# Performance work log

Measured on AMD Instinct MI355X. Metric: run time of the kernel, lower is better.

The kernel has to match this reference:

```python
import jax, jax.numpy as jnp
import numpy as np

N_NODES = 100000
N_EDGES = 640000
D = 128
EPS = 1e-5

def _full_layer_norm(x):
    # torch layer_norm with normalized_shape == x.shape: stats over ALL elements
    mu = jnp.mean(x)
    var = jnp.mean(jnp.square(x - mu))  # biased variance
    return (x - mu) * jax.lax.rsqrt(var + EPS)

def setup_inputs() -> dict:
    key = jax.random.key(0)
    k1, k2, k3, k4, k5 = jax.random.split(key, 5)
    scale1 = 1.0 / np.sqrt(D)
    scale2 = 1.0 / np.sqrt(2 * D)
    return {
        "edge_features": jax.random.normal(k1, (N_EDGES, D), dtype=jnp.float32),
        "node_features": jax.random.normal(k2, (N_NODES, D), dtype=jnp.float32),
        "edge_indices": jax.random.randint(k3, (N_EDGES, 2), 0, N_NODES, dtype=jnp.int32),
        "W1": jax.random.normal(k4, (D, D), dtype=jnp.float32) * scale1,
        "b1": jnp.zeros((D,), dtype=jnp.float32),
        "W2": jax.random.normal(k5, (2 * D, D), dtype=jnp.float32) * scale2,
        "b2": jnp.zeros((D,), dtype=jnp.float32),
    }

def reference(edge_features, node_features, edge_indices, W1, b1, W2, b2):
    # node MLP: linear -> whole-tensor layernorm -> gelu
    h = node_features @ W1 + b1                       # [N, D]
    h = jax.nn.gelu(_full_layer_norm(h), approximate=False)
    # gather source-node features onto edges
    src = edge_indices[:, 0]
    dst = edge_indices[:, 1]
    gathered = h[src]                                 # [E, D]
    e = jnp.concatenate([edge_features, gathered], axis=1)  # [E, 2D]
    e = e @ W2 + b2                                   # [E, D]
    e = jax.nn.gelu(_full_layer_norm(e), approximate=False)
    # scatter-mean (include_self=False): nodes with no in-edges stay 0
    seg_sum = jax.ops.segment_sum(e, dst, num_segments=N_NODES)       # [N, D]
    counts = jax.ops.segment_sum(jnp.ones((e.shape[0],), e.dtype), dst,
                                 num_segments=N_NODES)                 # [N]
    counts = counts[:, None]
    return jnp.where(counts > 0, seg_sum / jnp.maximum(counts, 1.0), 0.0)
```

## Files before the change

### kernel.cpp

```cpp
#include <hip/hip_runtime.h>
#include <hip/hip_bf16.h>
#include <math.h>

typedef __bf16 bf16;
typedef bf16 bf16x8 __attribute__((ext_vector_type(8)));
typedef float f32x4 __attribute__((ext_vector_type(4)));
typedef unsigned short ushort_t;
typedef unsigned long long u64;

#define N_NODES 100000
#define N_EDGES 640000
#define DD 128
#define MAXDEG 64
#define STAT_SCALE 1048576.0

__device__ __forceinline__ float gelu_fast(float x) {
    float z2 = x * (1.595769122f + 0.071354816f * x * x);
    return x * __builtin_amdgcn_rcpf(1.0f + __expf(-z2));
}

__device__ __forceinline__ ushort_t bf16_bits(float x) {
    bf16 h = (bf16)x;
    return __builtin_bit_cast(ushort_t, h);
}

__device__ __forceinline__ float bits_to_f(ushort_t u) {
    return __uint_as_float(((unsigned)u) << 16);
}

__device__ __forceinline__ long long to_fixed(double x) {
    return (long long)(x * STAT_SCALE + (x >= 0.0 ? 0.5 : -0.5));
}

__device__ __forceinline__ void stats_atomic(float lsum, float lsq, float* red,
                                             u64* dsum, u64* dsq) {
    int tid = threadIdx.x;
    red[tid] = lsum; __syncthreads();
    for (int s = 128; s > 0; s >>= 1) { if (tid < s) red[tid] += red[tid + s]; __syncthreads(); }
    float bs = red[0]; __syncthreads();
    red[tid] = lsq; __syncthreads();
    for (int s = 128; s > 0; s >>= 1) { if (tid < s) red[tid] += red[tid + s]; __syncthreads(); }
    if (tid == 0) {
        atomicAdd(dsum, (u64)to_fixed((double)bs));
        atomicAdd(dsq,  (u64)to_fixed((double)red[0]));
    }
}

__device__ __forceinline__ void stats_decode(const u64* stats, double cnt,
                                             float* mu, float* rs) {
    long long ss = (long long)stats[0], sq = (long long)stats[1];
    double mu_d = ((double)ss / STAT_SCALE) / cnt;
    double var  = ((double)sq / STAT_SCALE) / cnt - mu_d * mu_d;
    *mu = (float)mu_d;
    *rs = (float)(1.0 / sqrt(var + 1e-5));
}

#define K1_TILES 1563
__global__ __launch_bounds__(256) void k1_gemm1(
    const float* __restrict__ nf, const float* __restrict__ W1,
    const float* __restrict__ b1, ushort_t* __restrict__ hpre,
    u64* __restrict__ stats, int nblocks)
{
    __shared__ bf16 Ash[64 * 136];
    __shared__ float red[256];
    const int tid = threadIdx.x;
    const int lane = tid & 63;
    const int w = tid >> 6;
    const int l15 = lane & 15, l4 = lane >> 4;

    bf16x8 bfrag[4][2];
    #pragma unroll
    for (int s = 0; s < 4; ++s)
        #pragma unroll
        for (int t = 0; t < 2; ++t) {
            int n = w * 32 + t * 16 + l15;
            #pragma unroll
            for (int j = 0; j < 8; ++j)
                bfrag[s][t][j] = (bf16)W1[(s * 32 + l4 * 8 + j) * DD + n];
        }
    float4 bias4[2];
    bias4[0] = *(const float4*)&b1[w * 32 + l4 * 4];
    bias4[1] = *(const float4*)&b1[w * 32 + 16 + l4 * 4];

    float lsum = 0.f, lsq = 0.f;
    const int srow = tid >> 2;
    const int q = tid & 3;

    for (int tile = blockIdx.x; tile < K1_TILES; tile += nblocks) {
        const int rbase = tile * 64;
        {
            int grow = min(rbase + srow, N_NODES - 1);
            const float4* p = (const float4*)&nf[(size_t)grow * DD + q * 32];
            #pragma unroll
            for (int u = 0; u < 4; ++u) {
                float4 a = p[2 * u], b = p[2 * u + 1];
                ushort_t o[8] = {bf16_bits(a.x), bf16_bits(a.y), bf16_bits(a.z), bf16_bits(a.w),
                                 bf16_bits(b.x), bf16_bits(b.y), bf16_bits(b.z), bf16_bits(b.w)};
                *(uint4*)&Ash[srow * 136 + q * 32 + u * 8] = *(const uint4*)o;
            }
        }
        __syncthreads();
        f32x4 acc[4][2];
        #pragma unroll
        for (int r = 0; r < 4; ++r)
            #pragma unroll
            for (int t = 0; t < 2; ++t)
                acc[r][t] = (f32x4){0.f, 0.f, 0.f, 0.f};
        #pragma unroll
        for (int s = 0; s < 4; ++s)
            #pragma unroll
            for (int r = 0; r < 4; ++r) {
                bf16x8 a = *(const bf16x8*)&Ash[(r * 16 + l15) * 136 + s * 32 + l4 * 8];
                acc[r][0] = __builtin_amdgcn_mfma_f32_16x16x32_bf16(bfrag[s][0], a, acc[r][0], 0, 0, 0);
                acc[r][1] = __builtin_amdgcn_mfma_f32_16x16x32_bf16(bfrag[s][1], a, acc[r][1], 0, 0, 0);
            }
        __syncthreads();
        #pragma unroll
        for (int r = 0; r < 4; ++r) {
            int row = rbase + r * 16 + l15;
            if (row < N_NODES) {
                #pragma unroll
                for (int t = 0; t < 2; ++t) {
                    int col = w * 32 + t * 16 + l4 * 4;
                    ushort_t o[4];
                    #pragma unroll
                    for (int j = 0; j < 4; ++j) {
                        float v = acc[r][t][j] + bias4[t][j];
                        lsum += v; lsq += v * v;
                        o[j] = bf16_bits(v);
                    }
                    *(uint2*)&hpre[(size_t)row * DD + col] = *(const uint2*)o;
                }
            }
        }
    }
    stats_atomic(lsum, lsq, red, &stats[0], &stats[1]);
}

__global__ __launch_bounds__(256) void k2b_gemmh(
    const ushort_t* __restrict__ hpre, const float* __restrict__ W2,
    const u64* __restrict__ stats, ushort_t* __restrict__ hh, int nblocks)
{
    __shared__ bf16 Ash[64 * 136];
    float mu, rs;
    stats_decode(stats, (double)N_NODES * DD, &mu, &rs);

    const int tid = threadIdx.x;
    const int lane = tid & 63;
    const int w = tid >> 6;
    const int l15 = lane & 15, l4 = lane >> 4;

    bf16x8 bfrag[4][2];
    #pragma unroll
    for (int s = 0; s < 4; ++s)
        #pragma unroll
        for (int t = 0; t < 2; ++t) {
            int n = w * 32 + t * 16 + l15;
            #pragma unroll
            for (int j = 0; j < 8; ++j)
                bfrag[s][t][j] = (bf16)W2[(DD + s * 32 + l4 * 8 + j) * DD + n];
        }

    const int srow = tid >> 2;
    const int q = tid & 3;

    for (int tile = blockIdx.x; tile < K1_TILES; tile += nblocks) {
        const int rbase = tile * 64;
        {
            int grow = min(rbase + srow, N_NODES - 1);
            const uint4* p = (const uint4*)&hpre[(size_t)grow * DD + q * 32];
            #pragma unroll
            for (int u = 0; u < 4; ++u) {
                uint4 v = p[u];
                const ushort_t* in = (const ushort_t*)&v;
                ushort_t o[8];
                #pragma unroll
                for (int j = 0; j < 8; ++j)
                    o[j] = bf16_bits(gelu_fast((bits_to_f(in[j]) - mu) * rs));
                *(uint4*)&Ash[srow * 136 + q * 32 + u * 8] = *(const uint4*)o;
            }
        }
        __syncthreads();
        f32x4 acc[4][2];
        #pragma unroll
        for (int r = 0; r < 4; ++r)
            #pragma unroll
            for (int t = 0; t < 2; ++t)
                acc[r][t] = (f32x4){0.f, 0.f, 0.f, 0.f};
        #pragma unroll
        for (int s = 0; s < 4; ++s)
            #pragma unroll
            for (int r = 0; r < 4; ++r) {
                bf16x8 a = *(const bf16x8*)&Ash[(r * 16 + l15) * 136 + s * 32 + l4 * 8];
                acc[r][0] = __builtin_amdgcn_mfma_f32_16x16x32_bf16(bfrag[s][0], a, acc[r][0], 0, 0, 0);
                acc[r][1] = __builtin_amdgcn_mfma_f32_16x16x32_bf16(bfrag[s][1], a, acc[r][1], 0, 0, 0);
            }
        __syncthreads();
        #pragma unroll
        for (int r = 0; r < 4; ++r) {
            int row = rbase + r * 16 + l15;
            if (row < N_NODES) {
                #pragma unroll
                for (int t = 0; t < 2; ++t) {
                    int col = w * 32 + t * 16 + l4 * 4;
                    ushort_t o[4];
                    #pragma unroll
                    for (int j = 0; j < 4; ++j)
                        o[j] = bf16_bits(acc[r][t][j]);
                    *(uint2*)&hh[(size_t)row * DD + col] = *(const uint2*)o;
                }
            }
        }
    }
}

__global__ __launch_bounds__(256) void k4_gemm2(
    const float* __restrict__ ef, const ushort_t* __restrict__ hh,
    const int* __restrict__ eidx, const float* __restrict__ W2,
    const float* __restrict__ b2, ushort_t* __restrict__ e0,
    u64* __restrict__ stats, int nblocks)
{
    __shared__ bf16 Ash[64 * 136];
    __shared__ int Ssrc[64];
    __shared__ float red[256];
    const int tid = threadIdx.x;
    const int lane = tid & 63;
    const int w = tid >> 6;
    const int l15 = lane & 15, l4 = lane >> 4;

    bf16x8 bfrag[4][2];
    #pragma unroll
    for (int s = 0; s < 4; ++s)
        #pragma unroll
        for (int t = 0; t < 2; ++t) {
            int n = w * 32 + t * 16 + l15;
            #pragma unroll
            for (int j = 0; j < 8; ++j)
                bfrag[s][t][j] = (bf16)W2[(s * 32 + l4 * 8 + j) * DD + n];
        }
    float4 bias4[2];
    bias4[0] = *(const float4*)&b2[w * 32 + l4 * 4];
    bias4[1] = *(const float4*)&b2[w * 32 + 16 + l4 * 4];

    float lsum = 0.f, lsq = 0.f;
    const int srow = tid >> 2;
    const int q = tid & 3;

    for (int tile = blockIdx.x; tile < N_EDGES / 64; tile += nblocks) {
        const int ebase = tile * 64;
        {
            const float4* p = (const float4*)&ef[(size_t)(ebase + srow) * DD + q * 32];
            #pragma unroll
            for (int u = 0; u < 4; ++u) {
                float4 a = p[2 * u], b = p[2 * u + 1];
                ushort_t o[8] = {bf16_bits(a.x), bf16_bits(a.y), bf16_bits(a.z), bf16_bits(a.w),
                                 bf16_bits(b.x), bf16_bits(b.y), bf16_bits(b.z), bf16_bits(b.w)};
                *(uint4*)&Ash[srow * 136 + q * 32 + u * 8] = *(const uint4*)o;
            }
            if (tid < 64) Ssrc[tid] = eidx[(size_t)(ebase + tid) * 2];
        }
        __syncthreads();
        f32x4 acc[4][2];
        #pragma unroll
        for (int r = 0; r < 4; ++r)
            #pragma unroll
            for (int t = 0; t < 2; ++t)
                acc[r][t] = (f32x4){0.f, 0.f, 0.f, 0.f};
        #pragma unroll
        for (int s = 0; s < 4; ++s)
            #pragma unroll
            for (int r = 0; r < 4; ++r) {
                bf16x8 a = *(const bf16x8*)&Ash[(r * 16 + l15) * 136 + s * 32 + l4 * 8];
                acc[r][0] = __builtin_amdgcn_mfma_f32_16x16x32_bf16(bfrag[s][0], a, acc[r][0], 0, 0, 0);
                acc[r][1] = __builtin_amdgcn_mfma_f32_16x16x32_bf16(bfrag[s][1], a, acc[r][1], 0, 0, 0);
            }
        int srows[4];
        #pragma unroll
        for (int r = 0; r < 4; ++r) srows[r] = Ssrc[r * 16 + l15];
        __syncthreads();
        #pragma unroll
        for (int r = 0; r < 4; ++r) {
            int row = ebase + r * 16 + l15;
            #pragma unroll
            for (int t = 0; t < 2; ++t) {
                int col = w * 32 + t * 16 + l4 * 4;
                uint2 hv = *(const uint2*)&hh[(size_t)srows[r] * DD + col];
                float h0 = bits_to_f((ushort_t)(hv.x & 0xffff));
                float h1 = bits_to_f((ushort_t)(hv.x >> 16));
                float h2 = bits_to_f((ushort_t)(hv.y & 0xffff));
                float h3 = bits_to_f((ushort_t)(hv.y >> 16));
                float hadd[4] = {h0, h1, h2, h3};
                ushort_t o[4];
                #pragma unroll
                for (int j = 0; j < 4; ++j) {
                    float v = acc[r][t][j] + bias4[t][j] + hadd[j];
                    lsum += v; lsq += v * v;
                    o[j] = bf16_bits(v);
                }
                *(uint2*)&e0[(size_t)row * DD + col] = *(const uint2*)o;
            }
        }
    }
    stats_atomic(lsum, lsq, red, &stats[2], &stats[3]);
}

__global__ __launch_bounds__(256) void k7_fill(
    const int* __restrict__ eidx, int* __restrict__ cnt, int* __restrict__ slot)
{
    int e = blockIdx.x * 256 + threadIdx.x;
    if (e >= N_EDGES) return;
    int dst = eidx[(size_t)e * 2 + 1];
    int pos = atomicAdd(&cnt[dst], 1);
    if (pos < MAXDEG) slot[dst * MAXDEG + pos] = e;
}

__global__ __launch_bounds__(256) void k8_gather(
    const ushort_t* __restrict__ e0v, const int* __restrict__ slot,
    const int* __restrict__ cnt, const u64* __restrict__ stats,
    float* __restrict__ out)
{
    float mu, rs;
    stats_decode(stats + 2, (double)N_EDGES * DD, &mu, &rs);
    int node = (int)((blockIdx.x * 256 + threadIdx.x) >> 6);
    int lane = threadIdx.x & 63;
    if (node >= N_NODES) return;
    int c = cnt[node];
    int m = min(c, MAXDEG);
    int myslot = (lane < m) ? slot[node * MAXDEG + lane] : 0;
    float a0 = 0.f, a1 = 0.f;
    const size_t off = (size_t)(lane * 2);
    int j = 0;
    for (; j + 4 <= m; j += 4) {
        int ea = __shfl(myslot, j);
        int eb = __shfl(myslot, j + 1);
        int ec = __shfl(myslot, j + 2);
        int ed = __shfl(myslot, j + 3);
        unsigned ua = *(const unsigned*)&e0v[(size_t)ea * DD + off];
        unsigned ub = *(const unsigned*)&e0v[(size_t)eb * DD + off];
        unsigned uc = *(const unsigned*)&e0v[(size_t)ec * DD + off];
        unsigned ud = *(const unsigned*)&e0v[(size_t)ed * DD + off];
        a0 += gelu_fast((__uint_as_float(ua << 16) - mu) * rs);
        a1 += gelu_fast((__uint_as_float(ua & 0xffff0000u) - mu) * rs);
        a0 += gelu_fast((__uint_as_float(ub << 16) - mu) * rs);
        a1 += gelu_fast((__uint_as_float(ub & 0xffff0000u) - mu) * rs);
        a0 += gelu_fast((__uint_as_float(uc << 16) - mu) * rs);
        a1 += gelu_fast((__uint_as_float(uc & 0xffff0000u) - mu) * rs);
        a0 += gelu_fast((__uint_as_float(ud << 16) - mu) * rs);
        a1 += gelu_fast((__uint_as_float(ud & 0xffff0000u) - mu) * rs);
    }
    for (; j < m; ++j) {
        int ea = __shfl(myslot, j);
        unsigned ua = *(const unsigned*)&e0v[(size_t)ea * DD + off];
        a0 += gelu_fast((__uint_as_float(ua << 16) - mu) * rs);
        a1 += gelu_fast((__uint_as_float(ua & 0xffff0000u) - mu) * rs);
    }
    float inv = c > 0 ? 1.0f / (float)c : 0.f;
    float2 res = {a0 * inv, a1 * inv};
    *(float2*)&out[(size_t)node * DD + lane * 2] = res;
}

extern "C" void kernel_launch(void* const* d_in, const int* in_sizes, int n_in,
                              void* d_out, int out_size, void* d_ws, size_t ws_size,
                              hipStream_t stream) {
    const float* ef  = (const float*)d_in[0];
    const float* nf  = (const float*)d_in[1];
    const int*   eix = (const int*)d_in[2];
    const float* W1  = (const float*)d_in[3];
    const float* b1  = (const float*)d_in[4];
    const float* W2  = (const float*)d_in[5];
    const float* b2  = (const float*)d_in[6];
    float* out = (float*)d_out;
    char* ws = (char*)d_ws;

    ushort_t* hpre  = (ushort_t*)(ws + 0);
    ushort_t* hh    = (ushort_t*)(ws + 25600000);
    ushort_t* e0    = (ushort_t*)(ws + 51200000);
    int*      cnt   = (int*)(ws + 215040000);
    u64*      stats = (u64*)(ws + 215440000);
    int*      slot  = (int*)(ws + 215440064);

    hipMemsetAsync(cnt, 0, 400064, stream);
    k1_gemm1<<<782, 256, 0, stream>>>(nf, W1, b1, hpre, stats, 782);
    k2b_gemmh<<<782, 256, 0, stream>>>(hpre, W2, stats, hh, 782);
    k7_fill<<<2500, 256, 0, stream>>>(eix, cnt, slot);
    k4_gemm2<<<2500, 256, 0, stream>>>(ef, hh, eix, W2, b2, e0, stats, 2500);
    k8_gather<<<25000, 256, 0, stream>>>(e0, slot, cnt, stats, out);
}
```

Measured before the change: 311.3 us.

## Register-prefetch next tile in GEMM kernels and hoist gather loads

The three GEMM kernels now software-pipeline their input tiles: the next tile's rows are loaded into registers while the current tile runs through MFMA, then packed into shared memory at the top of the next iteration. In k4, the source-index and hh-gather loads are issued at the start of each tile instead of after the MFMA loop, so their latency can overlap with compute. Grid sizes are reduced so each block processes several tiles and the prefetch has work to overlap with. The cost is extra register pressure from the prefetch buffers and fewer resident blocks.

New measurement: 302.0 us. 1.03x faster.

```diff
diff --git a/kernel.cpp b/kernel.cpp
--- a/kernel.cpp
+++ b/kernel.cpp
@@ -54,6 +54,11 @@
     *mu = (float)mu_d;
     *rs = (float)(1.0 / sqrt(var + 1e-5));
 }
+
+#define PACK8(dstp, a, b) { \
+    ushort_t o_[8] = {bf16_bits(a.x), bf16_bits(a.y), bf16_bits(a.z), bf16_bits(a.w), \
+                      bf16_bits(b.x), bf16_bits(b.y), bf16_bits(b.z), bf16_bits(b.w)}; \
+    *(uint4*)(dstp) = *(const uint4*)o_; }
 
 #define K1_TILES 1563
 __global__ __launch_bounds__(256) void k1_gemm1(
@@ -86,20 +91,28 @@
     const int srow = tid >> 2;
     const int q = tid & 3;
 
+    float4 efr[8];
+    {
+        int grow = min(blockIdx.x * 64 + srow, N_NODES - 1);
+        const float4* p = (const float4*)&nf[(size_t)grow * DD + q * 32];
+        #pragma unroll
+        for (int u = 0; u < 8; ++u) efr[u] = p[u];
+    }
+
     for (int tile = blockIdx.x; tile < K1_TILES; tile += nblocks) {
         const int rbase = tile * 64;
-        {
-            int grow = min(rbase + srow, N_NODES - 1);
+        __syncthreads();
+        #pragma unroll
+        for (int u = 0; u < 4; ++u)
+            PACK8(&Ash[srow * 136 + q * 32 + u * 8], efr[2 * u], efr[2 * u + 1]);
+        __syncthreads();
+        int nt = tile + nblocks;
+        if (nt < K1_TILES) {
+            int grow = min(nt * 64 + srow, N_NODES - 1);
             const float4* p = (const float4*)&nf[(size_t)grow * DD + q * 32];
             #pragma unroll
-            for (int u = 0; u < 4; ++u) {
-                float4 a = p[2 * u], b = p[2 * u + 1];
-                ushort_t o[8] = {bf16_bits(a.x), bf16_bits(a.y), bf16_bits(a.z), bf16_bits(a.w),
-                                 bf16_bits(b.x), bf16_bits(b.y), bf16_bits(b.z), bf16_bits(b.w)};
-                *(uint4*)&Ash[srow * 136 + q * 32 + u * 8] = *(const uint4*)o;
-            }
-        }
-        __syncthreads();
+            for (int u = 0; u < 8; ++u) efr[u] = p[u];
+        }
         f32x4 acc[4][2];
         #pragma unroll
         for (int r = 0; r < 4; ++r)
@@ -114,7 +127,6 @@
                 acc[r][0] = __builtin_amdgcn_mfma_f32_16x16x32_bf16(bfrag[s][0], a, acc[r][0], 0, 0, 0);
                 acc[r][1] = __builtin_amdgcn_mfma_f32_16x16x32_bf16(bfrag[s][1], a, acc[r][1], 0, 0, 0);
             }
-        __syncthreads();
         #pragma unroll
         for (int r = 0; r < 4; ++r) {
             int row = rbase + r * 16 + l15;
@@ -164,23 +176,34 @@
     const int srow = tid >> 2;
     const int q = tid & 3;
 
+    uint4 hr[4];
+    {
+        int grow = min(blockIdx.x * 64 + srow, N_NODES - 1);
+        const uint4* p = (const uint4*)&hpre[(size_t)grow * DD + q * 32];
+        #pragma unroll
+        for (int u = 0; u < 4; ++u) hr[u] = p[u];
+    }
+
     for (int tile = blockIdx.x; tile < K1_TILES; tile += nblocks) {
         const int rbase = tile * 64;
-        {
-            int grow = min(rbase + srow, N_NODES - 1);
+        __syncthreads();
+        #pragma unroll
+        for (int u = 0; u < 4; ++u) {
+            const ushort_t* in = (const ushort_t*)&hr[u];
+            ushort_t o[8];
+            #pragma unroll
+            for (int j = 0; j < 8; ++j)
+                o[j] = bf16_bits(gelu_fast((bits_to_f(in[j]) - mu) * rs));
+            *(uint4*)&Ash[srow * 136 + q * 32 + u * 8] = *(const uint4*)o;
+        }
+        __syncthreads();
+        int nt = tile + nblocks;
+        if (nt < K1_TILES) {
+            int grow = min(nt * 64 + srow, N_NODES - 1);
             const uint4* p = (const uint4*)&hpre[(size_t)grow * DD + q * 32];
             #pragma unroll
-            for (int u = 0; u < 4; ++u) {
-                uint4 v = p[u];
-                const ushort_t* in = (const ushort_t*)&v;
-                ushort_t o[8];
-                #pragma unroll
-                for (int j = 0; j < 8; ++j)
-                    o[j] = bf16_bits(gelu_fast((bits_to_f(in[j]) - mu) * rs));
-                *(uint4*)&Ash[srow * 136 + q * 32 + u * 8] = *(const uint4*)o;
-            }
-        }
-        __syncthreads();
+            for (int u = 0; u < 4; ++u) hr[u] = p[u];
+        }
         f32x4 acc[4][2];
         #pragma unroll
         for (int r = 0; r < 4; ++r)
@@ -195,7 +218,6 @@
                 acc[r][0] = __builtin_amdgcn_mfma_f32_16x16x32_bf16(bfrag[s][0], a, acc[r][0], 0, 0, 0);
                 acc[r][1] = __builtin_amdgcn_mfma_f32_16x16x32_bf16(bfrag[s][1], a, acc[r][1], 0, 0, 0);
             }
-        __syncthreads();
         #pragma unroll
         for (int r = 0; r < 4; ++r) {
             int row = rbase + r * 16 + l15;
@@ -214,6 +236,7 @@
     }
 }
 
+#define K4_TILES (N_EDGES / 64)
 __global__ __launch_bounds__(256) void k4_gemm2(
     const float* __restrict__ ef, const ushort_t* __restrict__ hh,
     const int* __restrict__ eidx, const float* __restrict__ W2,
@@ -221,7 +244,6 @@
     u64* __restrict__ stats, int nblocks)
 {
     __shared__ bf16 Ash[64 * 136];
-    __shared__ int Ssrc[64];
     __shared__ float red[256];
     const int tid = threadIdx.x;
     const int lane = tid & 63;
@@ -246,20 +268,36 @@
     const int srow = tid >> 2;
     const int q = tid & 3;
 
-    for (int tile = blockIdx.x; tile < N_EDGES / 64; tile += nblocks) {
+    float4 efr[8];
+    {
+        const float4* p = (const float4*)&ef[(size_t)(blockIdx.x * 64 + srow) * DD + q * 32];
+        #pragma unroll
+        for (int u = 0; u < 8; ++u) efr[u] = p[u];
+    }
+
+    for (int tile = blockIdx.x; tile < K4_TILES; tile += nblocks) {
         const int ebase = tile * 64;
-        {
-            const float4* p = (const float4*)&ef[(size_t)(ebase + srow) * DD + q * 32];
-            #pragma unroll
-            for (int u = 0; u < 4; ++u) {
-                float4 a = p[2 * u], b = p[2 * u + 1];
-                ushort_t o[8] = {bf16_bits(a.x), bf16_bits(a.y), bf16_bits(a.z), bf16_bits(a.w),
-                                 bf16_bits(b.x), bf16_bits(b.y), bf16_bits(b.z), bf16_bits(b.w)};
-                *(uint4*)&Ash[srow * 136 + q * 32 + u * 8] = *(const uint4*)o;
-            }
-            if (tid < 64) Ssrc[tid] = eidx[(size_t)(ebase + tid) * 2];
-        }
-        __syncthreads();
+        int srcv[4];
+        #pragma unroll
+        for (int r = 0; r < 4; ++r)
+            srcv[r] = eidx[(size_t)(ebase + r * 16 + l15) * 2];
+        uint2 hv[4][2];
+        #pragma unroll
+        for (int r = 0; r < 4; ++r)
+            #pragma unroll
+            for (int t = 0; t < 2; ++t)
+                hv[r][t] = *(const uint2*)&hh[(size_t)srcv[r] * DD + w * 32 + t * 16 + l4 * 4];
+        __syncthreads();
+        #pragma unroll
+        for (int u = 0; u < 4; ++u)
+            PACK8(&Ash[srow * 136 + q * 32 + u * 8], efr[2 * u], efr[2 * u + 1]);
+        __syncthreads();
+        int nt = tile + nblocks;
+        if (nt < K4_TILES) {
+            const float4* p = (const float4*)&ef[(size_t)(nt * 64 + srow) * DD + q * 32];
+            #pragma unroll
+            for (int u = 0; u < 8; ++u) efr[u] = p[u];
+        }
         f32x4 acc[4][2];
         #pragma unroll
         for (int r = 0; r < 4; ++r)
@@ -274,22 +312,16 @@
                 acc[r][0] = __builtin_amdgcn_mfma_f32_16x16x32_bf16(bfrag[s][0], a, acc[r][0], 0, 0, 0);
                 acc[r][1] = __builtin_amdgcn_mfma_f32_16x16x32_bf16(bfrag[s][1], a, acc[r][1], 0, 0, 0);
             }
-        int srows[4];
-        #pragma unroll
-        for (int r = 0; r < 4; ++r) srows[r] = Ssrc[r * 16 + l15];
-        __syncthreads();
         #pragma unroll
         for (int r = 0; r < 4; ++r) {
             int row = ebase + r * 16 + l15;
             #pragma unroll
             for (int t = 0; t < 2; ++t) {
                 int col = w * 32 + t * 16 + l4 * 4;
-                uint2 hv = *(const uint2*)&hh[(size_t)srows[r] * DD + col];
-                float h0 = bits_to_f((ushort_t)(hv.x & 0xffff));
-                float h1 = bits_to_f((ushort_t)(hv.x >> 16));
-                float h2 = bits_to_f((ushort_t)(hv.y & 0xffff));
-                float h3 = bits_to_f((ushort_t)(hv.y >> 16));
-                float hadd[4] = {h0, h1, h2, h3};
+                float hadd[4] = {bits_to_f((ushort_t)(hv[r][t].x & 0xffff)),
+                                 bits_to_f((ushort_t)(hv[r][t].x >> 16)),
+                                 bits_to_f((ushort_t)(hv[r][t].y & 0xffff)),
+                                 bits_to_f((ushort_t)(hv[r][t].y >> 16))};
                 ushort_t o[4];
                 #pragma unroll
                 for (int j = 0; j < 4; ++j) {
@@ -380,9 +412,9 @@
     int*      slot  = (int*)(ws + 215440064);
 
     hipMemsetAsync(cnt, 0, 400064, stream);
-    k1_gemm1<<<782, 256, 0, stream>>>(nf, W1, b1, hpre, stats, 782);
-    k2b_gemmh<<<782, 256, 0, stream>>>(hpre, W2, stats, hh, 782);
+    k1_gemm1<<<521, 256, 0, stream>>>(nf, W1, b1, hpre, stats, 521);
+    k2b_gemmh<<<521, 256, 0, stream>>>(hpre, W2, stats, hh, 521);
     k7_fill<<<2500, 256, 0, stream>>>(eix, cnt, slot);
-    k4_gemm2<<<2500, 256, 0, stream>>>(ef, hh, eix, W2, b2, e0, stats, 2500);
+    k4_gemm2<<<1250, 256, 0, stream>>>(ef, hh, eix, W2, b2, e0, stats, 1250);
     k8_gather<<<25000, 256, 0, stream>>>(e0, slot, cnt, stats, out);
 }
```
